# Kernel optimization log

Hardware: AMD Instinct MI355X
Metric: run time of the kernel (lower is better)

The kernel has to match this reference:

```python
import jax, jax.numpy as jnp
import numpy as np

N = 50000   # nodes
E = 800000  # edges (avg degree 16)
F = 96      # num_features
H = 96      # hidden_channels
G = 64      # graphs in batch
ALPHA = 0.5


def setup_inputs() -> dict:
    key = jax.random.key(0)
    ks = jax.random.split(key, 32)
    inp = {
        "x": jax.random.normal(ks[0], (N, F), jnp.float32),
        "edge_index": jax.random.randint(ks[1], (2, E), 0, N, dtype=jnp.int32),
        "batch": jnp.sort(jax.random.randint(ks[2], (N,), 0, G, dtype=jnp.int32)),
    }
    i = 3
    dims = [(F, H), (H, H), (H, H)]
    for l, (din, dout) in enumerate(dims, start=1):
        for tag in ("Wself", "Wsd", "Wds"):
            inp[f"{tag}{l}"] = jax.random.normal(ks[i], (din, dout), jnp.float32) * 0.05; i += 1
        for tag in ("bself", "bsd", "bds"):
            inp[f"{tag}{l}"] = jax.random.normal(ks[i], (dout,), jnp.float32) * 0.05; i += 1
    inp["lin1_w"] = jax.random.normal(ks[i], (H, 5), jnp.float32) * 0.05; i += 1
    inp["lin1_b"] = jax.random.normal(ks[i], (5,), jnp.float32) * 0.05; i += 1
    inp["lin2_w"] = jax.random.normal(ks[i], (5, 1), jnp.float32) * 0.05; i += 1
    inp["lin2_b"] = jax.random.normal(ks[i], (1,), jnp.float32) * 0.05
    return inp


def _agg_mean(x, idx_from, idx_to, n):
    # scatter-mean of x[idx_from] onto idx_to (PyG SAGEConv mean aggregation;
    # nodes with no incoming edges get 0)
    s = jax.ops.segment_sum(x[idx_from], idx_to, num_segments=n)
    c = jax.ops.segment_sum(jnp.ones((idx_to.shape[0],), x.dtype), idx_to, num_segments=n)
    return s / jnp.maximum(c, 1.0)[:, None]


def _dir_sage(x, src, dst, Wself, bself, Wsd, bsd, Wds, bds):
    n = x.shape[0]
    out_self = x @ Wself + bself
    # source_to_target: aggregate x[src] at dst; target_to_source: aggregate x[dst] at src
    out_sd = _agg_mean(x, src, dst, n) @ Wsd + bsd
    out_ds = _agg_mean(x, dst, src, n) @ Wds + bds
    return out_self + (1.0 - ALPHA) * out_sd + ALPHA * out_ds


def reference(x, edge_index, batch,
              Wself1, bself1, Wsd1, bsd1, Wds1, bds1,
              Wself2, bself2, Wsd2, bsd2, Wds2, bds2,
              Wself3, bself3, Wsd3, bsd3, Wds3, bds3,
              lin1_w, lin1_b, lin2_w, lin2_b):
    src, dst = edge_index[0], edge_index[1]
    h = jax.nn.relu(_dir_sage(x, src, dst, Wself1, bself1, Wsd1, bsd1, Wds1, bds1))
    h = jax.nn.relu(_dir_sage(h, src, dst, Wself2, bself2, Wsd2, bsd2, Wds2, bds2))
    h = jax.nn.relu(_dir_sage(h, src, dst, Wself3, bself3, Wsd3, bsd3, Wds3, bds3))
    g = jax.ops.segment_max(h, batch, num_segments=G)  # global_max_pool -> [G, H]
    g = jax.nn.relu(g @ lin1_w + lin1_b)
    return g @ lin2_w + lin2_b  # [G, 1]
```

## Files before the change

### kernel.cpp

```cpp
#include <hip/hip_runtime.h>
#include <hip/hip_bf16.h>

#define HF 96
#define GG 64
#define SB 64

typedef __attribute__((ext_vector_type(8))) short bf16x8;
typedef __attribute__((ext_vector_type(4))) float f32x4;

__device__ __forceinline__ unsigned short f2bf(float f) {
    unsigned u = __float_as_uint(f);
    unsigned r = (u + 0x7FFFu + ((u >> 16) & 1u)) >> 16;
    return (unsigned short)r;
}
__device__ __forceinline__ float bf2f(unsigned short h) {
    return __uint_as_float(((unsigned)h) << 16);
}

__global__ void count_kernel(const int* __restrict__ ei, int* __restrict__ cnt_dst,
                             int* __restrict__ cnt_src, int* __restrict__ slot_d,
                             int* __restrict__ slot_s, int E) {
    int e = blockIdx.x * blockDim.x + threadIdx.x;
    if (e >= E) return;
    int s = ei[e];
    int d = ei[E + e];
    slot_d[e] = atomicAdd(&cnt_dst[d], 1);
    slot_s[e] = atomicAdd(&cnt_src[s], 1);
}

__global__ __launch_bounds__(256) void scan_phase1(const int* __restrict__ cnt0,
                                                   const int* __restrict__ cnt1,
                                                   int* __restrict__ off0,
                                                   int* __restrict__ off1,
                                                   int* __restrict__ bsum, int N, int CH) {
    int dir = blockIdx.y;
    const int* cnt = dir ? cnt1 : cnt0;
    int* off = dir ? off1 : off0;
    int base = blockIdx.x * CH;
    int end = base + CH; if (end > N) end = N;
    __shared__ int buf[256];
    int carry = 0;
    for (int s = base; s < end; s += 256) {
        int i = s + threadIdx.x;
        int v = (i < end) ? cnt[i] : 0;
        buf[threadIdx.x] = v;
        __syncthreads();
        for (int st = 1; st < 256; st <<= 1) {
            int tv = (threadIdx.x >= st) ? buf[threadIdx.x - st] : 0;
            __syncthreads();
            buf[threadIdx.x] += tv;
            __syncthreads();
        }
        if (i < end) off[i] = carry + buf[threadIdx.x] - v;
        carry += buf[255];
        __syncthreads();
    }
    if (threadIdx.x == 0) bsum[dir * SB + blockIdx.x] = carry;
}

__global__ __launch_bounds__(64) void scan_phase2(int* __restrict__ bsum, int* __restrict__ boff,
                                                  int* __restrict__ off0, int* __restrict__ off1,
                                                  int N) {
    int dir = blockIdx.x;
    __shared__ int buf[SB];
    int v = bsum[dir * SB + threadIdx.x];
    buf[threadIdx.x] = v;
    __syncthreads();
    for (int st = 1; st < SB; st <<= 1) {
        int tv = (threadIdx.x >= st) ? buf[threadIdx.x - st] : 0;
        __syncthreads();
        buf[threadIdx.x] += tv;
        __syncthreads();
    }
    boff[dir * SB + threadIdx.x] = buf[threadIdx.x] - v;
    if (threadIdx.x == SB - 1) {
        int* off = dir ? off1 : off0;
        off[N] = buf[SB - 1];
    }
}

__global__ void scan_phase3(int* __restrict__ off0, int* __restrict__ off1,
                            const int* __restrict__ boff, int N, int CH) {
    int dir = blockIdx.y;
    int* off = dir ? off1 : off0;
    int i = blockIdx.x * 256 + threadIdx.x;
    if (i >= N) return;
    off[i] += boff[dir * SB + i / CH];
}

__global__ void fill_kernel(const int* __restrict__ ei, const int* __restrict__ off_dst,
                            const int* __restrict__ off_src, const int* __restrict__ slot_d,
                            const int* __restrict__ slot_s, int* __restrict__ nbr_dst,
                            int* __restrict__ nbr_src, int E) {
    int e = blockIdx.x * blockDim.x + threadIdx.x;
    if (e >= E) return;
    int s = ei[e];
    int d = ei[E + e];
    nbr_dst[off_dst[d] + slot_d[e]] = s;
    nbr_src[off_src[s] + slot_s[e]] = d;
}

__global__ void prep_kernel(const float* __restrict__ Wself, const float* __restrict__ Wsd,
                            const float* __restrict__ Wds, const float* __restrict__ bself,
                            const float* __restrict__ bsd, const float* __restrict__ bds,
                            unsigned short* __restrict__ Whi, unsigned short* __restrict__ Wlo,
                            float* __restrict__ bc) {
    int idx = blockIdx.x * 256 + threadIdx.x;
    if (idx < HF * 288) {
        int j = idx / 288;
        int kk = idx % 288;
        int m = kk / HF, k = kk % HF;
        const float* W = (m == 0) ? Wself : (m == 1) ? Wsd : Wds;
        float w = W[k * HF + j];
        unsigned short hi = f2bf(w);
        float rem = w - bf2f(hi);
        Whi[idx] = hi;
        Wlo[idx] = f2bf(rem);
    } else if (idx < HF * 288 + HF) {
        int j = idx - HF * 288;
        bc[j] = bself[j] + 0.5f * (bsd[j] + bds[j]);
    }
}

__global__ __launch_bounds__(256) void gather_kernel(
        const float* __restrict__ x,
        const int* __restrict__ off_dst, const int* __restrict__ nbr_dst,
        const int* __restrict__ off_src, const int* __restrict__ nbr_src,
        float* __restrict__ agg_sd, float* __restrict__ agg_ds, int N) {
    int t = blockIdx.x * blockDim.x + threadIdx.x;
    int n2 = t / 24;
    if (n2 >= 2 * N) return;
    int q = t % 24;
    int dir = (n2 >= N) ? 1 : 0;
    int n = n2 - dir * N;
    const int* off = dir ? off_src : off_dst;
    const int* nbr = dir ? nbr_src : nbr_dst;
    float* agg = dir ? agg_ds : agg_sd;

    int b = off[n], e = off[n + 1];
    const float* xq = x + q * 4;
    float4 a0 = make_float4(0.f, 0.f, 0.f, 0.f);
    float4 a1 = make_float4(0.f, 0.f, 0.f, 0.f);
    float4 a2 = make_float4(0.f, 0.f, 0.f, 0.f);
    float4 a3 = make_float4(0.f, 0.f, 0.f, 0.f);
    int i = b;
    for (; i + 4 <= e; i += 4) {
        int i0 = nbr[i + 0], i1 = nbr[i + 1], i2 = nbr[i + 2], i3 = nbr[i + 3];
        float4 v0 = *(const float4*)(xq + (long long)i0 * HF);
        float4 v1 = *(const float4*)(xq + (long long)i1 * HF);
        float4 v2 = *(const float4*)(xq + (long long)i2 * HF);
        float4 v3 = *(const float4*)(xq + (long long)i3 * HF);
        a0.x += v0.x; a0.y += v0.y; a0.z += v0.z; a0.w += v0.w;
        a1.x += v1.x; a1.y += v1.y; a1.z += v1.z; a1.w += v1.w;
        a2.x += v2.x; a2.y += v2.y; a2.z += v2.z; a2.w += v2.w;
        a3.x += v3.x; a3.y += v3.y; a3.z += v3.z; a3.w += v3.w;
    }
    for (; i < e; i++) {
        int i0 = nbr[i];
        float4 v0 = *(const float4*)(xq + (long long)i0 * HF);
        a0.x += v0.x; a0.y += v0.y; a0.z += v0.z; a0.w += v0.w;
    }
    float4 acc;
    acc.x = (a0.x + a1.x) + (a2.x + a3.x);
    acc.y = (a0.y + a1.y) + (a2.y + a3.y);
    acc.z = (a0.z + a1.z) + (a2.z + a3.z);
    acc.w = (a0.w + a1.w) + (a2.w + a3.w);
    float inv = 0.5f / fmaxf((float)(e - b), 1.0f);
    acc.x *= inv; acc.y *= inv; acc.z *= inv; acc.w *= inv;
    *(float4*)(agg + (long long)n * HF + q * 4) = acc;
}

#define LPAD 40
__global__ __launch_bounds__(256) void sage_mfma(
        const float* __restrict__ x, const float* __restrict__ agg_sd,
        const float* __restrict__ agg_ds,
        const unsigned short* __restrict__ Whi_g, const unsigned short* __restrict__ Wlo_g,
        const float* __restrict__ bc,
        float* __restrict__ out, int N) {
    __shared__ __align__(16) unsigned short Ahi[64 * LPAD];
    __shared__ __align__(16) unsigned short Alo[64 * LPAD];
    __shared__ __align__(16) unsigned short Whi[96 * LPAD];
    __shared__ __align__(16) unsigned short Wlo[96 * LPAD];

    const int tx = threadIdx.x;
    const int lane = tx & 63;
    const int wid = tx >> 6;
    const int wr = (wid >> 1) * 32;
    const int wc = (wid & 1) * 48;
    const int m = lane & 15;
    const int quad = lane >> 4;
    const int row0 = blockIdx.x * 64;

    const int arow = tx >> 2;
    const int aq = tx & 3;
    int argc = row0 + arow; if (argc > N - 1) argc = N - 1;

    f32x4 acc[2][3];
#pragma unroll
    for (int rt = 0; rt < 2; rt++)
#pragma unroll
        for (int ct = 0; ct < 3; ct++) acc[rt][ct] = (f32x4){0.f, 0.f, 0.f, 0.f};

    for (int kt = 0; kt < 9; kt++) {
        const float* A = (kt < 3) ? x : (kt < 6) ? agg_sd : agg_ds;
        const int koff = (kt % 3) * 32;
        const int kglob = kt * 32;

        {
            const float* Ar = A + (long long)argc * HF + koff + aq * 8;
            float4 v0 = *(const float4*)(Ar + 0);
            float4 v1 = *(const float4*)(Ar + 4);
            float f[8] = {v0.x, v0.y, v0.z, v0.w, v1.x, v1.y, v1.z, v1.w};
            bf16x8 hv, lv;
#pragma unroll
            for (int i = 0; i < 8; i++) {
                unsigned short h = f2bf(f[i]);
                hv[i] = (short)h;
                lv[i] = (short)f2bf(f[i] - bf2f(h));
            }
            *(bf16x8*)&Ahi[arow * LPAD + aq * 8] = hv;
            *(bf16x8*)&Alo[arow * LPAD + aq * 8] = lv;
        }
        for (int s = tx; s < 384; s += 256) {
            int n = s >> 2, q2 = s & 3;
            long long go = (long long)n * 288 + kglob + q2 * 8;
            *(bf16x8*)&Whi[n * LPAD + q2 * 8] = *(const bf16x8*)(Whi_g + go);
            *(bf16x8*)&Wlo[n * LPAD + q2 * 8] = *(const bf16x8*)(Wlo_g + go);
        }
        __syncthreads();

        bf16x8 ah[2], al[2], bh[3], bl[3];
#pragma unroll
        for (int rt = 0; rt < 2; rt++) {
            int r = (wr + rt * 16 + m) * LPAD + quad * 8;
            ah[rt] = *(const bf16x8*)&Ahi[r];
            al[rt] = *(const bf16x8*)&Alo[r];
        }
#pragma unroll
        for (int ct = 0; ct < 3; ct++) {
            int r = (wc + ct * 16 + m) * LPAD + quad * 8;
            bh[ct] = *(const bf16x8*)&Whi[r];
            bl[ct] = *(const bf16x8*)&Wlo[r];
        }
#pragma unroll
        for (int rt = 0; rt < 2; rt++)
#pragma unroll
            for (int ct = 0; ct < 3; ct++) {
                acc[rt][ct] = __builtin_amdgcn_mfma_f32_16x16x32_bf16(ah[rt], bh[ct], acc[rt][ct], 0, 0, 0);
                acc[rt][ct] = __builtin_amdgcn_mfma_f32_16x16x32_bf16(ah[rt], bl[ct], acc[rt][ct], 0, 0, 0);
                acc[rt][ct] = __builtin_amdgcn_mfma_f32_16x16x32_bf16(al[rt], bh[ct], acc[rt][ct], 0, 0, 0);
            }
        __syncthreads();
    }

#pragma unroll
    for (int ct = 0; ct < 3; ct++) {
        int col = wc + ct * 16 + m;
        float bcv = bc[col];
#pragma unroll
        for (int rt = 0; rt < 2; rt++) {
#pragma unroll
            for (int reg = 0; reg < 4; reg++) {
                int r = row0 + wr + rt * 16 + quad * 4 + reg;
                if (r < N) out[(long long)r * HF + col] = fmaxf(acc[rt][ct][reg] + bcv, 0.f);
            }
        }
    }
}

#define POOL_CHUNK 128
__global__ void pool_kernel(const float* __restrict__ h, const int* __restrict__ batch,
                            unsigned* __restrict__ g, int N) {
    int j = threadIdx.x;
    if (j >= HF) return;
    int n0 = blockIdx.x * POOL_CHUNK;
    int end = n0 + POOL_CHUNK;
    if (end > N) end = N;
    float cur = 0.0f;
    int curb = -1;
    for (int n = n0; n < end; n++) {
        int b = batch[n];
        float v = h[(long long)n * HF + j];
        if (b != curb) {
            if (curb >= 0) atomicMax(&g[curb * HF + j], __float_as_uint(cur));
            curb = b;
            cur = v;
        } else {
            cur = fmaxf(cur, v);
        }
    }
    if (curb >= 0) atomicMax(&g[curb * HF + j], __float_as_uint(cur));
}

__global__ void mlp_kernel(const unsigned* __restrict__ g, const float* __restrict__ lin1_w,
                           const float* __restrict__ lin1_b, const float* __restrict__ lin2_w,
                           const float* __restrict__ lin2_b, float* __restrict__ out) {
    int gi = threadIdx.x;
    if (gi >= GG) return;
    float h5[5];
#pragma unroll
    for (int hh = 0; hh < 5; hh++) {
        float acc = lin1_b[hh];
#pragma unroll 8
        for (int k = 0; k < HF; k++)
            acc = fmaf(__uint_as_float(g[gi * HF + k]), lin1_w[k * 5 + hh], acc);
        h5[hh] = fmaxf(acc, 0.0f);
    }
    float o = lin2_b[0];
#pragma unroll
    for (int hh = 0; hh < 5; hh++) o = fmaf(h5[hh], lin2_w[hh * 1 + 0], o);
    out[gi] = o;
}

extern "C" void kernel_launch(void* const* d_in, const int* in_sizes, int n_in,
                              void* d_out, int out_size, void* d_ws, size_t ws_size,
                              hipStream_t stream) {
    const float* x     = (const float*)d_in[0];
    const int*   ei    = (const int*)d_in[1];
    const int*   batch = (const int*)d_in[2];
    const float* W[3][3];
    const float* B[3][3];
    for (int l = 0; l < 3; l++) {
        for (int t = 0; t < 3; t++) W[l][t] = (const float*)d_in[3 + l * 6 + t];
        for (int t = 0; t < 3; t++) B[l][t] = (const float*)d_in[3 + l * 6 + 3 + t];
    }
    const float* lin1_w = (const float*)d_in[21];
    const float* lin1_b = (const float*)d_in[22];
    const float* lin2_w = (const float*)d_in[23];
    const float* lin2_b = (const float*)d_in[24];

    const int N = in_sizes[0] / HF;
    const int E = in_sizes[1] / 2;

    float* hA      = (float*)d_ws;
    float* hB      = hA + (long long)N * HF;
    float* agg_sd  = hB + (long long)N * HF;
    float* agg_ds  = agg_sd + (long long)N * HF;
    int*   cnt_dst = (int*)(agg_ds + (long long)N * HF);
    int*   cnt_src = cnt_dst + N;
    int*   off_dst = cnt_src + N;
    int*   off_src = off_dst + (N + 1);
    int*   nbr_dst = off_src + (N + 1);
    int*   nbr_src = nbr_dst + E;
    int*   slot_d  = nbr_src + E;
    int*   slot_s  = slot_d + E;
    int*   bsum    = slot_s + E;
    int*   boff    = bsum + 2 * SB;
    float* bc3     = (float*)(boff + 2 * SB);
    uintptr_t p = (uintptr_t)(bc3 + 3 * HF);
    p = (p + 15) & ~(uintptr_t)15;
    unsigned short* Whi3 = (unsigned short*)p;
    unsigned short* Wlo3 = Whi3 + 3 * HF * 288;
    uintptr_t p2 = (uintptr_t)(Wlo3 + 3 * HF * 288);
    p2 = (p2 + 15) & ~(uintptr_t)15;
    unsigned* g = (unsigned*)p2;

    hipMemsetAsync(cnt_dst, 0, (size_t)2 * N * sizeof(int), stream);
    hipMemsetAsync(g, 0, (size_t)GG * HF * sizeof(unsigned), stream);

    const int prep_blocks = (HF * 288 + HF + 255) / 256;
    for (int l = 0; l < 3; l++)
        prep_kernel<<<prep_blocks, 256, 0, stream>>>(
            W[l][0], W[l][1], W[l][2], B[l][0], B[l][1], B[l][2],
            Whi3 + (long long)l * HF * 288, Wlo3 + (long long)l * HF * 288, bc3 + l * HF);

    const int CH = (N + SB - 1) / SB;
    count_kernel<<<(E + 255) / 256, 256, 0, stream>>>(ei, cnt_dst, cnt_src, slot_d, slot_s, E);
    scan_phase1<<<dim3(SB, 2), 256, 0, stream>>>(cnt_dst, cnt_src, off_dst, off_src, bsum, N, CH);
    scan_phase2<<<2, SB, 0, stream>>>(bsum, boff, off_dst, off_src, N);
    scan_phase3<<<dim3((N + 255) / 256, 2), 256, 0, stream>>>(off_dst, off_src, boff, N, CH);
    fill_kernel<<<(E + 255) / 256, 256, 0, stream>>>(ei, off_dst, off_src,
                                                     slot_d, slot_s, nbr_dst, nbr_src, E);

    const long long gather_threads = (long long)2 * N * 24;
    const int gather_blocks = (int)((gather_threads + 255) / 256);
    const int gemm_blocks = (N + 63) / 64;
    const int pool_blocks = (N + POOL_CHUNK - 1) / POOL_CHUNK;

    const float* cur_in = x;
    float* outs[3] = { hA, hB, hA };
    for (int l = 0; l < 3; l++) {
        gather_kernel<<<gather_blocks, 256, 0, stream>>>(
            cur_in, off_dst, nbr_dst, off_src, nbr_src, agg_sd, agg_ds, N);
        sage_mfma<<<gemm_blocks, 256, 0, stream>>>(
            cur_in, agg_sd, agg_ds,
            Whi3 + (long long)l * HF * 288, Wlo3 + (long long)l * HF * 288,
            bc3 + l * HF, outs[l], N);
        cur_in = outs[l];
    }

    pool_kernel<<<pool_blocks, 128, 0, stream>>>(outs[2], batch, g, N);
    mlp_kernel<<<1, 64, 0, stream>>>(g, lin1_w, lin1_b, lin2_w, lin2_b, (float*)d_out);
}
```

Before: 559.2 us.

## Store node features in 8 column slabs so gathers stay cache-resident

Node features are now kept in a slab layout: 8 slabs of 12 floats per node. Each gather block handles a single slab, so the randomly indexed neighbour reads touch a working set of about 2.4 MB instead of the full 19 MB feature matrix, which should improve L2 hit rates. The GEMM reads x from the slab layout and, for the first two layers, writes its output back in slab layout. An extra slab conversion kernel runs on the input, each neighbour list is now read once per slab, and GEMM stores become strided.

```diff
diff --git a/kernel.cpp b/kernel.cpp
--- a/kernel.cpp
+++ b/kernel.cpp
@@ -122,23 +122,37 @@
     }
 }
 
+__global__ __launch_bounds__(256) void slab_kernel(const float* __restrict__ x,
+                                                   float* __restrict__ xg, int N) {
+    int t = blockIdx.x * 256 + threadIdx.x;
+    int n = t / 24, q = t % 24;
+    if (n >= N) return;
+    float4 v = *(const float4*)(x + (long long)n * HF + q * 4);
+    int s = q / 3, c = q % 3;
+    *(float4*)(xg + ((long long)s * N + n) * 12 + c * 4) = v;
+}
+
+#define PPB 85
 __global__ __launch_bounds__(256) void gather_kernel(
-        const float* __restrict__ x,
+        const float* __restrict__ xg,
         const int* __restrict__ off_dst, const int* __restrict__ nbr_dst,
         const int* __restrict__ off_src, const int* __restrict__ nbr_src,
         float* __restrict__ agg_sd, float* __restrict__ agg_ds, int N) {
-    int t = blockIdx.x * blockDim.x + threadIdx.x;
-    int n2 = t / 24;
-    if (n2 >= 2 * N) return;
-    int q = t % 24;
-    int dir = (n2 >= N) ? 1 : 0;
-    int n = n2 - dir * N;
+    int slice = blockIdx.x & 7;
+    int grp = blockIdx.x >> 3;
+    int tp = threadIdx.x / 3;
+    int c = threadIdx.x % 3;
+    if (tp >= PPB) return;
+    int P = grp * PPB + tp;
+    if (P >= 2 * N) return;
+    int dir = (P >= N) ? 1 : 0;
+    int n = P - dir * N;
     const int* off = dir ? off_src : off_dst;
     const int* nbr = dir ? nbr_src : nbr_dst;
     float* agg = dir ? agg_ds : agg_sd;
 
     int b = off[n], e = off[n + 1];
-    const float* xq = x + q * 4;
+    const float* xq = xg + (long long)slice * N * 12 + c * 4;
     float4 a0 = make_float4(0.f, 0.f, 0.f, 0.f);
     float4 a1 = make_float4(0.f, 0.f, 0.f, 0.f);
     float4 a2 = make_float4(0.f, 0.f, 0.f, 0.f);
@@ -146,10 +160,10 @@
     int i = b;
     for (; i + 4 <= e; i += 4) {
         int i0 = nbr[i + 0], i1 = nbr[i + 1], i2 = nbr[i + 2], i3 = nbr[i + 3];
-        float4 v0 = *(const float4*)(xq + (long long)i0 * HF);
-        float4 v1 = *(const float4*)(xq + (long long)i1 * HF);
-        float4 v2 = *(const float4*)(xq + (long long)i2 * HF);
-        float4 v3 = *(const float4*)(xq + (long long)i3 * HF);
+        float4 v0 = *(const float4*)(xq + (long long)i0 * 12);
+        float4 v1 = *(const float4*)(xq + (long long)i1 * 12);
+        float4 v2 = *(const float4*)(xq + (long long)i2 * 12);
+        float4 v3 = *(const float4*)(xq + (long long)i3 * 12);
         a0.x += v0.x; a0.y += v0.y; a0.z += v0.z; a0.w += v0.w;
         a1.x += v1.x; a1.y += v1.y; a1.z += v1.z; a1.w += v1.w;
         a2.x += v2.x; a2.y += v2.y; a2.z += v2.z; a2.w += v2.w;
@@ -157,7 +171,7 @@
     }
     for (; i < e; i++) {
         int i0 = nbr[i];
-        float4 v0 = *(const float4*)(xq + (long long)i0 * HF);
+        float4 v0 = *(const float4*)(xq + (long long)i0 * 12);
         a0.x += v0.x; a0.y += v0.y; a0.z += v0.z; a0.w += v0.w;
     }
     float4 acc;
@@ -167,16 +181,16 @@
     acc.w = (a0.w + a1.w) + (a2.w + a3.w);
     float inv = 0.5f / fmaxf((float)(e - b), 1.0f);
     acc.x *= inv; acc.y *= inv; acc.z *= inv; acc.w *= inv;
-    *(float4*)(agg + (long long)n * HF + q * 4) = acc;
+    *(float4*)(agg + (long long)n * HF + slice * 12 + c * 4) = acc;
 }
 
 #define LPAD 40
 __global__ __launch_bounds__(256) void sage_mfma(
-        const float* __restrict__ x, const float* __restrict__ agg_sd,
+        const float* __restrict__ xg, const float* __restrict__ agg_sd,
         const float* __restrict__ agg_ds,
         const unsigned short* __restrict__ Whi_g, const unsigned short* __restrict__ Wlo_g,
         const float* __restrict__ bc,
-        float* __restrict__ out, int N) {
+        float* __restrict__ out, int slab_out, int N) {
     __shared__ __align__(16) unsigned short Ahi[64 * LPAD];
     __shared__ __align__(16) unsigned short Alo[64 * LPAD];
     __shared__ __align__(16) unsigned short Whi[96 * LPAD];
@@ -202,14 +216,24 @@
         for (int ct = 0; ct < 3; ct++) acc[rt][ct] = (f32x4){0.f, 0.f, 0.f, 0.f};
 
     for (int kt = 0; kt < 9; kt++) {
-        const float* A = (kt < 3) ? x : (kt < 6) ? agg_sd : agg_ds;
         const int koff = (kt % 3) * 32;
         const int kglob = kt * 32;
 
         {
-            const float* Ar = A + (long long)argc * HF + koff + aq * 8;
-            float4 v0 = *(const float4*)(Ar + 0);
-            float4 v1 = *(const float4*)(Ar + 4);
+            float4 v0, v1;
+            const int c0 = koff + aq * 8;
+            if (kt < 3) {
+                int s0i = c0 / 12, r0 = c0 % 12;
+                int c1 = c0 + 4;
+                int s1i = c1 / 12, r1 = c1 % 12;
+                v0 = *(const float4*)(xg + ((long long)s0i * N + argc) * 12 + r0);
+                v1 = *(const float4*)(xg + ((long long)s1i * N + argc) * 12 + r1);
+            } else {
+                const float* A = (kt < 6) ? agg_sd : agg_ds;
+                const float* Ar = A + (long long)argc * HF + c0;
+                v0 = *(const float4*)(Ar + 0);
+                v1 = *(const float4*)(Ar + 4);
+            }
             float f[8] = {v0.x, v0.y, v0.z, v0.w, v1.x, v1.y, v1.z, v1.w};
             bf16x8 hv, lv;
 #pragma unroll
@@ -257,12 +281,25 @@
     for (int ct = 0; ct < 3; ct++) {
         int col = wc + ct * 16 + m;
         float bcv = bc[col];
-#pragma unroll
-        for (int rt = 0; rt < 2; rt++) {
-#pragma unroll
-            for (int reg = 0; reg < 4; reg++) {
-                int r = row0 + wr + rt * 16 + quad * 4 + reg;
-                if (r < N) out[(long long)r * HF + col] = fmaxf(acc[rt][ct][reg] + bcv, 0.f);
+        if (slab_out) {
+            int sidx = col / 12, cc = col % 12;
+            float* base = out + (long long)sidx * N * 12 + cc;
+#pragma unroll
+            for (int rt = 0; rt < 2; rt++) {
+#pragma unroll
+                for (int reg = 0; reg < 4; reg++) {
+                    int r = row0 + wr + rt * 16 + quad * 4 + reg;
+                    if (r < N) base[(long long)r * 12] = fmaxf(acc[rt][ct][reg] + bcv, 0.f);
+                }
+            }
+        } else {
+#pragma unroll
+            for (int rt = 0; rt < 2; rt++) {
+#pragma unroll
+                for (int reg = 0; reg < 4; reg++) {
+                    int r = row0 + wr + rt * 16 + quad * 4 + reg;
+                    if (r < N) out[(long long)r * HF + col] = fmaxf(acc[rt][ct][reg] + bcv, 0.f);
+                }
             }
         }
     }
@@ -331,12 +368,13 @@
 
     const int N = in_sizes[0] / HF;
     const int E = in_sizes[1] / 2;
-
-    float* hA      = (float*)d_ws;
-    float* hB      = hA + (long long)N * HF;
-    float* agg_sd  = hB + (long long)N * HF;
-    float* agg_ds  = agg_sd + (long long)N * HF;
-    int*   cnt_dst = (int*)(agg_ds + (long long)N * HF);
+    const long long NH = (long long)N * HF;
+
+    float* s0      = (float*)d_ws;
+    float* s1      = s0 + NH;
+    float* agg_sd  = s1 + NH;
+    float* agg_ds  = agg_sd + NH;
+    int*   cnt_dst = (int*)(agg_ds + NH);
     int*   cnt_src = cnt_dst + N;
     int*   off_dst = cnt_src + N;
     int*   off_src = off_dst + (N + 1);
@@ -364,6 +402,8 @@
             W[l][0], W[l][1], W[l][2], B[l][0], B[l][1], B[l][2],
             Whi3 + (long long)l * HF * 288, Wlo3 + (long long)l * HF * 288, bc3 + l * HF);
 
+    slab_kernel<<<(int)((NH / 4 + 255) / 256), 256, 0, stream>>>(x, s0, N);
+
     const int CH = (N + SB - 1) / SB;
     count_kernel<<<(E + 255) / 256, 256, 0, stream>>>(ei, cnt_dst, cnt_src, slot_d, slot_s, E);
     scan_phase1<<<dim3(SB, 2), 256, 0, stream>>>(cnt_dst, cnt_src, off_dst, off_src, bsum, N, CH);
@@ -372,23 +412,22 @@
     fill_kernel<<<(E + 255) / 256, 256, 0, stream>>>(ei, off_dst, off_src,
                                                      slot_d, slot_s, nbr_dst, nbr_src, E);
 
-    const long long gather_threads = (long long)2 * N * 24;
-    const int gather_blocks = (int)((gather_threads + 255) / 256);
+    const int bps = (2 * N + PPB - 1) / PPB;
+    const int gather_blocks = bps * 8;
     const int gemm_blocks = (N + 63) / 64;
     const int pool_blocks = (N + POOL_CHUNK - 1) / POOL_CHUNK;
 
-    const float* cur_in = x;
-    float* outs[3] = { hA, hB, hA };
+    const float* slab_in[3] = { s0, s1, s0 };
+    float*       outp[3]    = { s1, s0, s1 };
     for (int l = 0; l < 3; l++) {
         gather_kernel<<<gather_blocks, 256, 0, stream>>>(
-            cur_in, off_dst, nbr_dst, off_src, nbr_src, agg_sd, agg_ds, N);
+            slab_in[l], off_dst, nbr_dst, off_src, nbr_src, agg_sd, agg_ds, N);
         sage_mfma<<<gemm_blocks, 256, 0, stream>>>(
-            cur_in, agg_sd, agg_ds,
+            slab_in[l], agg_sd, agg_ds,
             Whi3 + (long long)l * HF * 288, Wlo3 + (long long)l * HF * 288,
-            bc3 + l * HF, outs[l], N);
-        cur_in = outs[l];
-    }
-
-    pool_kernel<<<pool_blocks, 128, 0, stream>>>(outs[2], batch, g, N);
+            bc3 + l * HF, outp[l], (l < 2) ? 1 : 0, N);
+    }
+
+    pool_kernel<<<pool_blocks, 128, 0, stream>>>(s1, batch, g, N);
     mlp_kernel<<<1, 64, 0, stream>>>(g, lin1_w, lin1_b, lin2_w, lin2_b, (float*)d_out);
 }
```

New measurement: 657.0 us. 1.17x slower.

## Store activations and aggregates in interleaved bf16 hi/lo split layout

Applied to the files above, without the earlier changes.

Activations, the source-to-target aggregate and the target-to-source aggregate now share one workspace row of 576 bf16 values, each stored as interleaved hi/lo bf16 pairs. The GEMM no longer does the fp32-to-split-bf16 conversion per tile and just copies the packed words into shared memory. The epilogue stages results through shared memory so it writes coalesced packed rows, or fp32 for the last layer. Gather reads the same 16 bytes per 4 features but reconstructs fp32 from the hi+lo parts. This adds an xprep kernel and slightly changes precision, since the aggregates are accumulated from split values.

```diff
diff --git a/kernel.cpp b/kernel.cpp
--- a/kernel.cpp
+++ b/kernel.cpp
@@ -7,6 +7,7 @@
 
 typedef __attribute__((ext_vector_type(8))) short bf16x8;
 typedef __attribute__((ext_vector_type(4))) float f32x4;
+typedef unsigned int uint;
 
 __device__ __forceinline__ unsigned short f2bf(float f) {
     unsigned u = __float_as_uint(f);
@@ -15,6 +16,25 @@
 }
 __device__ __forceinline__ float bf2f(unsigned short h) {
     return __uint_as_float(((unsigned)h) << 16);
+}
+
+__device__ __forceinline__ uint4 pack_hilo4(float f0, float f1, float f2, float f3) {
+    unsigned short h0 = f2bf(f0), h1 = f2bf(f1), h2 = f2bf(f2), h3 = f2bf(f3);
+    unsigned short l0 = f2bf(f0 - bf2f(h0)), l1 = f2bf(f1 - bf2f(h1));
+    unsigned short l2 = f2bf(f2 - bf2f(h2)), l3 = f2bf(f3 - bf2f(h3));
+    uint4 o;
+    o.x = (uint)h0 | ((uint)h1 << 16);
+    o.y = (uint)h2 | ((uint)h3 << 16);
+    o.z = (uint)l0 | ((uint)l1 << 16);
+    o.w = (uint)l2 | ((uint)l3 << 16);
+    return o;
+}
+
+__device__ __forceinline__ void acc_hilo4(float4& a, uint4 w) {
+    a.x += __uint_as_float(w.x << 16) + __uint_as_float(w.z << 16);
+    a.y += __uint_as_float(w.x & 0xFFFF0000u) + __uint_as_float(w.z & 0xFFFF0000u);
+    a.z += __uint_as_float(w.y << 16) + __uint_as_float(w.w << 16);
+    a.w += __uint_as_float(w.y & 0xFFFF0000u) + __uint_as_float(w.w & 0xFFFF0000u);
 }
 
 __global__ void count_kernel(const int* __restrict__ ei, int* __restrict__ cnt_dst,
@@ -122,11 +142,19 @@
     }
 }
 
+__global__ __launch_bounds__(256) void xprep_kernel(const float* __restrict__ x,
+                                                    unsigned short* __restrict__ Ag, int N) {
+    int t = blockIdx.x * 256 + threadIdx.x;
+    int n = t / 24, q = t % 24;
+    if (n >= N) return;
+    float4 v = *(const float4*)(x + (long long)n * HF + q * 4);
+    *(uint4*)(Ag + ((long long)n * 576 + q * 8)) = pack_hilo4(v.x, v.y, v.z, v.w);
+}
+
 __global__ __launch_bounds__(256) void gather_kernel(
-        const float* __restrict__ x,
+        unsigned short* Ag,
         const int* __restrict__ off_dst, const int* __restrict__ nbr_dst,
-        const int* __restrict__ off_src, const int* __restrict__ nbr_src,
-        float* __restrict__ agg_sd, float* __restrict__ agg_ds, int N) {
+        const int* __restrict__ off_src, const int* __restrict__ nbr_src, int N) {
     int t = blockIdx.x * blockDim.x + threadIdx.x;
     int n2 = t / 24;
     if (n2 >= 2 * N) return;
@@ -135,10 +163,9 @@
     int n = n2 - dir * N;
     const int* off = dir ? off_src : off_dst;
     const int* nbr = dir ? nbr_src : nbr_dst;
-    float* agg = dir ? agg_ds : agg_sd;
 
     int b = off[n], e = off[n + 1];
-    const float* xq = x + q * 4;
+    const unsigned short* xq = Ag + q * 8;
     float4 a0 = make_float4(0.f, 0.f, 0.f, 0.f);
     float4 a1 = make_float4(0.f, 0.f, 0.f, 0.f);
     float4 a2 = make_float4(0.f, 0.f, 0.f, 0.f);
@@ -146,19 +173,19 @@
     int i = b;
     for (; i + 4 <= e; i += 4) {
         int i0 = nbr[i + 0], i1 = nbr[i + 1], i2 = nbr[i + 2], i3 = nbr[i + 3];
-        float4 v0 = *(const float4*)(xq + (long long)i0 * HF);
-        float4 v1 = *(const float4*)(xq + (long long)i1 * HF);
-        float4 v2 = *(const float4*)(xq + (long long)i2 * HF);
-        float4 v3 = *(const float4*)(xq + (long long)i3 * HF);
-        a0.x += v0.x; a0.y += v0.y; a0.z += v0.z; a0.w += v0.w;
-        a1.x += v1.x; a1.y += v1.y; a1.z += v1.z; a1.w += v1.w;
-        a2.x += v2.x; a2.y += v2.y; a2.z += v2.z; a2.w += v2.w;
-        a3.x += v3.x; a3.y += v3.y; a3.z += v3.z; a3.w += v3.w;
+        uint4 w0 = *(const uint4*)(xq + (long long)i0 * 576);
+        uint4 w1 = *(const uint4*)(xq + (long long)i1 * 576);
+        uint4 w2 = *(const uint4*)(xq + (long long)i2 * 576);
+        uint4 w3 = *(const uint4*)(xq + (long long)i3 * 576);
+        acc_hilo4(a0, w0);
+        acc_hilo4(a1, w1);
+        acc_hilo4(a2, w2);
+        acc_hilo4(a3, w3);
     }
     for (; i < e; i++) {
         int i0 = nbr[i];
-        float4 v0 = *(const float4*)(xq + (long long)i0 * HF);
-        a0.x += v0.x; a0.y += v0.y; a0.z += v0.z; a0.w += v0.w;
+        uint4 w0 = *(const uint4*)(xq + (long long)i0 * 576);
+        acc_hilo4(a0, w0);
     }
     float4 acc;
     acc.x = (a0.x + a1.x) + (a2.x + a3.x);
@@ -167,20 +194,22 @@
     acc.w = (a0.w + a1.w) + (a2.w + a3.w);
     float inv = 0.5f / fmaxf((float)(e - b), 1.0f);
     acc.x *= inv; acc.y *= inv; acc.z *= inv; acc.w *= inv;
-    *(float4*)(agg + (long long)n * HF + q * 4) = acc;
+    int chunk = 24 + dir * 24 + q;
+    *(uint4*)(Ag + ((long long)n * 576 + chunk * 8)) = pack_hilo4(acc.x, acc.y, acc.z, acc.w);
 }
 
 #define LPAD 40
 __global__ __launch_bounds__(256) void sage_mfma(
-        const float* __restrict__ x, const float* __restrict__ agg_sd,
-        const float* __restrict__ agg_ds,
+        unsigned short* Ag,
         const unsigned short* __restrict__ Whi_g, const unsigned short* __restrict__ Wlo_g,
         const float* __restrict__ bc,
-        float* __restrict__ out, int N) {
-    __shared__ __align__(16) unsigned short Ahi[64 * LPAD];
-    __shared__ __align__(16) unsigned short Alo[64 * LPAD];
-    __shared__ __align__(16) unsigned short Whi[96 * LPAD];
-    __shared__ __align__(16) unsigned short Wlo[96 * LPAD];
+        float* __restrict__ h3, int mode, int N) {
+    __shared__ __align__(16) unsigned char POOL[25600];
+    unsigned short* Ahi = (unsigned short*)POOL;
+    unsigned short* Alo = Ahi + 64 * LPAD;
+    unsigned short* Whi = Alo + 64 * LPAD;
+    unsigned short* Wlo = Whi + 96 * LPAD;
+    float* C = (float*)POOL;
 
     const int tx = threadIdx.x;
     const int lane = tx & 63;
@@ -192,8 +221,9 @@
     const int row0 = blockIdx.x * 64;
 
     const int arow = tx >> 2;
-    const int aq = tx & 3;
+    const int aj = tx & 3;
     int argc = row0 + arow; if (argc > N - 1) argc = N - 1;
+    const unsigned short* Arow = Ag + (long long)argc * 576;
 
     f32x4 acc[2][3];
 #pragma unroll
@@ -202,24 +232,15 @@
         for (int ct = 0; ct < 3; ct++) acc[rt][ct] = (f32x4){0.f, 0.f, 0.f, 0.f};
 
     for (int kt = 0; kt < 9; kt++) {
-        const float* A = (kt < 3) ? x : (kt < 6) ? agg_sd : agg_ds;
-        const int koff = (kt % 3) * 32;
         const int kglob = kt * 32;
 
         {
-            const float* Ar = A + (long long)argc * HF + koff + aq * 8;
-            float4 v0 = *(const float4*)(Ar + 0);
-            float4 v1 = *(const float4*)(Ar + 4);
-            float f[8] = {v0.x, v0.y, v0.z, v0.w, v1.x, v1.y, v1.z, v1.w};
-            bf16x8 hv, lv;
-#pragma unroll
-            for (int i = 0; i < 8; i++) {
-                unsigned short h = f2bf(f[i]);
-                hv[i] = (short)h;
-                lv[i] = (short)f2bf(f[i] - bf2f(h));
-            }
-            *(bf16x8*)&Ahi[arow * LPAD + aq * 8] = hv;
-            *(bf16x8*)&Alo[arow * LPAD + aq * 8] = lv;
+            const uint4 v0 = *(const uint4*)(Arow + (kt * 8 + aj * 2 + 0) * 8);
+            const uint4 v1 = *(const uint4*)(Arow + (kt * 8 + aj * 2 + 1) * 8);
+            *(uint2*)&Ahi[arow * LPAD + aj * 8 + 0] = make_uint2(v0.x, v0.y);
+            *(uint2*)&Alo[arow * LPAD + aj * 8 + 0] = make_uint2(v0.z, v0.w);
+            *(uint2*)&Ahi[arow * LPAD + aj * 8 + 4] = make_uint2(v1.x, v1.y);
+            *(uint2*)&Alo[arow * LPAD + aj * 8 + 4] = make_uint2(v1.z, v1.w);
         }
         for (int s = tx; s < 384; s += 256) {
             int n = s >> 2, q2 = s & 3;
@@ -261,8 +282,32 @@
         for (int rt = 0; rt < 2; rt++) {
 #pragma unroll
             for (int reg = 0; reg < 4; reg++) {
-                int r = row0 + wr + rt * 16 + quad * 4 + reg;
-                if (r < N) out[(long long)r * HF + col] = fmaxf(acc[rt][ct][reg] + bcv, 0.f);
+                int rl = wr + rt * 16 + quad * 4 + reg;
+                C[rl * 100 + col] = fmaxf(acc[rt][ct][reg] + bcv, 0.f);
+            }
+        }
+    }
+    __syncthreads();
+
+    {
+        int rl = tx >> 2;
+        int r = row0 + rl;
+        if (r < N) {
+            if (mode == 0) {
+                unsigned short* Orow = Ag + (long long)r * 576;
+#pragma unroll
+                for (int k = 0; k < 6; k++) {
+                    int c = aj * 6 + k;
+                    const float* src = &C[rl * 100 + c * 4];
+                    *(uint4*)(Orow + c * 8) = pack_hilo4(src[0], src[1], src[2], src[3]);
+                }
+            } else {
+                float* Orow = h3 + (long long)r * HF;
+#pragma unroll
+                for (int k = 0; k < 6; k++) {
+                    int c = aj * 6 + k;
+                    *(float4*)(Orow + c * 4) = *(const float4*)&C[rl * 100 + c * 4];
+                }
             }
         }
     }
@@ -332,11 +377,9 @@
     const int N = in_sizes[0] / HF;
     const int E = in_sizes[1] / 2;
 
-    float* hA      = (float*)d_ws;
-    float* hB      = hA + (long long)N * HF;
-    float* agg_sd  = hB + (long long)N * HF;
-    float* agg_ds  = agg_sd + (long long)N * HF;
-    int*   cnt_dst = (int*)(agg_ds + (long long)N * HF);
+    unsigned short* Ag = (unsigned short*)d_ws;
+    float* h3      = (float*)(Ag + (long long)N * 576);
+    int*   cnt_dst = (int*)(h3 + (long long)N * HF);
     int*   cnt_src = cnt_dst + N;
     int*   off_dst = cnt_src + N;
     int*   off_src = off_dst + (N + 1);
@@ -364,6 +407,8 @@
             W[l][0], W[l][1], W[l][2], B[l][0], B[l][1], B[l][2],
             Whi3 + (long long)l * HF * 288, Wlo3 + (long long)l * HF * 288, bc3 + l * HF);
 
+    xprep_kernel<<<(N * 24 + 255) / 256, 256, 0, stream>>>(x, Ag, N);
+
     const int CH = (N + SB - 1) / SB;
     count_kernel<<<(E + 255) / 256, 256, 0, stream>>>(ei, cnt_dst, cnt_src, slot_d, slot_s, E);
     scan_phase1<<<dim3(SB, 2), 256, 0, stream>>>(cnt_dst, cnt_src, off_dst, off_src, bsum, N, CH);
@@ -377,18 +422,15 @@
     const int gemm_blocks = (N + 63) / 64;
     const int pool_blocks = (N + POOL_CHUNK - 1) / POOL_CHUNK;
 
-    const float* cur_in = x;
-    float* outs[3] = { hA, hB, hA };
     for (int l = 0; l < 3; l++) {
         gather_kernel<<<gather_blocks, 256, 0, stream>>>(
-            cur_in, off_dst, nbr_dst, off_src, nbr_src, agg_sd, agg_ds, N);
+            Ag, off_dst, nbr_dst, off_src, nbr_src, N);
         sage_mfma<<<gemm_blocks, 256, 0, stream>>>(
-            cur_in, agg_sd, agg_ds,
+            Ag,
             Whi3 + (long long)l * HF * 288, Wlo3 + (long long)l * HF * 288,
-            bc3 + l * HF, outs[l], N);
-        cur_in = outs[l];
-    }
-
-    pool_kernel<<<pool_blocks, 128, 0, stream>>>(outs[2], batch, g, N);
+            bc3 + l * HF, h3, (l < 2) ? 0 : 1, N);
+    }
+
+    pool_kernel<<<pool_blocks, 128, 0, stream>>>(h3, batch, g, N);
     mlp_kernel<<<1, 64, 0, stream>>>(g, lin1_w, lin1_b, lin2_w, lin2_b, (float*)d_out);
 }
```

New measurement: 581.1 us. 1.04x slower.
